# Kernel optimization log

Hardware: AMD Instinct MI355X
Metric: run time of the kernel (lower is better)

The kernel has to match this reference:

```python
import jax, jax.numpy as jnp
import numpy as np

L, H, NH, F = 6, 1024, 16, 4096
B, S = 4, 512
D = H // NH
LN_EPS = 1e-12
GELU_C = 0.7978845608028654  # sqrt(2/pi)


def gelu_new(x):
    return 0.5 * x * (1.0 + jnp.tanh(GELU_C * (x + 0.044715 * x * x * x)))


def layer_norm(x, ln):
    # ln: [2, H] -> gamma, beta
    m = jnp.mean(x, axis=-1, keepdims=True)
    v = jnp.mean(jnp.square(x - m), axis=-1, keepdims=True)
    return (x - m) * jax.lax.rsqrt(v + LN_EPS) * ln[0] + ln[1]


def attention(q_in, kv_in, mask, qkv_w, qkv_b):
    # qkv_w: [3, H, H], qkv_b: [3, H]; mask: [B, S_kv] (1 = keep)
    b, s_q, _ = q_in.shape
    s_kv = kv_in.shape[1]
    q = (q_in @ qkv_w[0] + qkv_b[0]).reshape(b, s_q, NH, D)
    k = (kv_in @ qkv_w[1] + qkv_b[1]).reshape(b, s_kv, NH, D)
    v = (kv_in @ qkv_w[2] + qkv_b[2]).reshape(b, s_kv, NH, D)
    scale = 1.0 / (D ** 0.5)
    score = jnp.einsum('bind,bjnd->bnij', q, k) * scale  # [B, NH, Sq, Skv]
    adder = (1.0 - mask.astype(score.dtype))[:, None, None, :] * -10000.0
    prob = jax.nn.softmax(score + adder, axis=-1)
    out = jnp.einsum('bnij,bjnd->bind', prob, v)
    return out.reshape(b, s_q, H)


def _forward(hidden_states, encoder_hidden_states, attention_mask, encoder_attention_mask,
             sa_qkv_w, sa_qkv_b, sa_out_w, sa_out_b, sa_ln,
             ca_qkv_w, ca_qkv_b, ca_out_w, ca_out_b, ca_ln,
             o1_w, o1_b, o1_ln, ffn_w, ffn_b, o2_w, o2_b, o2_ln):
    h = hidden_states
    for i in range(L):
        # self attention + dense/dropout/LN (residual = h)
        self_vec = attention(h, h, attention_mask, sa_qkv_w[i], sa_qkv_b[i])
        attn_out = layer_norm(self_vec @ sa_out_w[i] + sa_out_b[i] + h, sa_ln[i])
        # cross attention + dense/dropout/LN (residual = h, per original code)
        cross_vec = attention(h, encoder_hidden_states, encoder_attention_mask,
                              ca_qkv_w[i], ca_qkv_b[i])
        cross_out = layer_norm(cross_vec @ ca_out_w[i] + ca_out_b[i] + h, ca_ln[i])
        # output_1: dense(attn_out) + cross_out, then LN
        attn_out = layer_norm(attn_out @ o1_w[i] + o1_b[i] + cross_out, o1_ln[i])
        # FFN with gelu_new, output_2: dense(inter) + attn_out, then LN
        inter = gelu_new(attn_out @ ffn_w[i] + ffn_b[i])
        h = layer_norm(inter @ o2_w[i] + o2_b[i] + attn_out, o2_ln[i])
    return h


def setup_inputs() -> dict:
    key = jax.random.key(0)
    ks = jax.random.split(key, 16)
    std = 0.02
    w = lambda k, shape: (jax.random.normal(k, shape, jnp.float32) * std)
    ln_init = jnp.stack([jnp.ones((L, H), jnp.float32), jnp.zeros((L, H), jnp.float32)], axis=1)
    return {
        'hidden_states': jax.random.normal(ks[0], (B, S, H), jnp.float32),
        'encoder_hidden_states': jax.random.normal(ks[1], (B, S, H), jnp.float32),
        'attention_mask': jnp.ones((B, S), jnp.int32),
        'encoder_attention_mask': jnp.ones((B, S), jnp.int32),
        'sa_qkv_w': w(ks[2], (L, 3, H, H)), 'sa_qkv_b': w(ks[3], (L, 3, H)),
        'sa_out_w': w(ks[4], (L, H, H)), 'sa_out_b': w(ks[5], (L, H)), 'sa_ln': ln_init,
        'ca_qkv_w': w(ks[6], (L, 3, H, H)), 'ca_qkv_b': w(ks[7], (L, 3, H)),
        'ca_out_w': w(ks[8], (L, H, H)), 'ca_out_b': w(ks[9], (L, H)), 'ca_ln': ln_init,
        'o1_w': w(ks[10], (L, H, H)), 'o1_b': w(ks[11], (L, H)), 'o1_ln': ln_init,
        'ffn_w': w(ks[12], (L, H, F)), 'ffn_b': w(ks[13], (L, F)),
        'o2_w': w(ks[14], (L, F, H)), 'o2_b': w(ks[15], (L, H)), 'o2_ln': ln_init,
    }


def reference(hidden_states, encoder_hidden_states, attention_mask, encoder_attention_mask,
              sa_qkv_w, sa_qkv_b, sa_out_w, sa_out_b, sa_ln,
              ca_qkv_w, ca_qkv_b, ca_out_w, ca_out_b, ca_ln,
              o1_w, o1_b, o1_ln, ffn_w, ffn_b, o2_w, o2_b, o2_ln):
    return _forward(hidden_states, encoder_hidden_states, attention_mask, encoder_attention_mask,
                    sa_qkv_w, sa_qkv_b, sa_out_w, sa_out_b, sa_ln,
                    ca_qkv_w, ca_qkv_b, ca_out_w, ca_out_b, ca_ln,
                    o1_w, o1_b, o1_ln, ffn_w, ffn_b, o2_w, o2_b, o2_ln)
```

## Files before the change

kernel.cpp:

```cpp
#include <hip/hip_runtime.h>


#define LNUM 6
#define HDIM 1024
#define NHEAD 16
#define DHEAD 64
#define BDIM 4
#define SDIM 512
#define FDIM 4096
#define MROWS (BDIM * SDIM)
#define HSQ (HDIM * HDIM)

typedef __bf16 bf16_t;
typedef bf16_t bf16x8 __attribute__((ext_vector_type(8)));
typedef float f32x4 __attribute__((ext_vector_type(4)));

__device__ __forceinline__ float bf2f(unsigned short u) {
    union { unsigned int i; float f; } x;
    x.i = ((unsigned int)u) << 16;
    return x.f;
}

__device__ __forceinline__ unsigned short f2bf(float f) {
    union { float f; unsigned int i; } u;
    u.f = f;
    unsigned int x = u.i;
    unsigned int lsb = (x >> 16) & 1u;
    x += 0x7fffu + lsb;
    return (unsigned short)(x >> 16);
}

__device__ __forceinline__ void async16(const unsigned short* g, unsigned short* l) {
    __builtin_amdgcn_global_load_lds(
        (const __attribute__((address_space(1))) unsigned int*)g,
        (__attribute__((address_space(3))) unsigned int*)l, 16, 0, 0);
}

template<int N>
__device__ __forceinline__ void s_wait_vmcnt() {
    asm volatile("s_waitcnt vmcnt(%0)" :: "n"(N) : "memory");
}

template<int BM, int BN, bool GELU, bool OUTBF16>
__global__ __launch_bounds__(256) void mfma_gemm(
    const unsigned short* __restrict__ A,
    const unsigned short* __restrict__ BT,
    const float* __restrict__ bias,
    void* __restrict__ Cv,
    int M, int N, int K)
{
    constexpr int BK = 64;
    constexpr int MI = BM / 32;
    constexpr int NJ = BN / 32;
    constexpr int LPT = MI + NJ;

    __shared__ unsigned short As[3][BM][BK];
    __shared__ unsigned short Bs[3][BN][BK];

    const int t = threadIdx.x;
    const int w = t >> 6;
    const int lane = t & 63;
    const int quad = lane >> 4;
    const int cm = lane & 15;
    const int wrow = (w >> 1) * (BM / 2);
    const int wcol = (w & 1) * (BN / 2);
    const int row0 = blockIdx.x * BM;
    const int col0 = blockIdx.y * BN;

    f32x4 acc[MI][NJ] = {};

    const int lrow = lane >> 3;
    const int lcol = ((lane & 7) ^ lrow) * 8;
    const int sw = cm & 15 & 7;

    auto stage = [&](int buf, int k0) {
#pragma unroll
        for (int j = 0; j < BM / 32; ++j) {
            int mb = w * (BM / 4) + j * 8;
            async16(A + (size_t)(row0 + mb + lrow) * K + k0 + lcol, &As[buf][mb][0]);
        }
#pragma unroll
        for (int j = 0; j < BN / 32; ++j) {
            int nb = w * (BN / 4) + j * 8;
            async16(BT + (size_t)(col0 + nb + lrow) * K + k0 + lcol, &Bs[buf][nb][0]);
        }
    };

    const int NT = K / BK;
    stage(0, 0);
    stage(1, BK);
    int c0 = 0, c1 = 1, c2 = 2;
    for (int ti = 0; ti < NT; ++ti) {
        if (ti + 2 < NT) {
            stage(c2, (ti + 2) * BK);
            s_wait_vmcnt<2 * LPT>();
        } else if (ti + 1 < NT) {
            s_wait_vmcnt<LPT>();
        } else {
            s_wait_vmcnt<0>();
        }
        __builtin_amdgcn_s_barrier();
        __builtin_amdgcn_sched_barrier(0);

#pragma unroll
        for (int kk = 0; kk < BK; kk += 32) {
            const int cc = kk >> 3;
            bf16x8 av[MI], bv[NJ];
#pragma unroll
            for (int i = 0; i < MI; ++i)
                av[i] = *(const bf16x8*)&As[c0][wrow + 16 * i + cm][((cc + quad) ^ sw) * 8];
#pragma unroll
            for (int j = 0; j < NJ; ++j)
                bv[j] = *(const bf16x8*)&Bs[c0][wcol + 16 * j + cm][((cc + quad) ^ sw) * 8];
#pragma unroll
            for (int i = 0; i < MI; ++i)
#pragma unroll
                for (int j = 0; j < NJ; ++j)
                    acc[i][j] = __builtin_amdgcn_mfma_f32_16x16x32_bf16(
                        av[i], bv[j], acc[i][j], 0, 0, 0);
        }

        __builtin_amdgcn_sched_barrier(0);
        __builtin_amdgcn_s_barrier();
        int tmp = c0; c0 = c1; c1 = c2; c2 = tmp;
    }

#pragma unroll
    for (int j = 0; j < NJ; ++j) {
        int col = col0 + wcol + 16 * j + cm;
        float bb = bias[col];
#pragma unroll
        for (int i = 0; i < MI; ++i) {
#pragma unroll
            for (int r = 0; r < 4; ++r) {
                int row = row0 + wrow + 16 * i + quad * 4 + r;
                float c = acc[i][j][r] + bb;
                if (GELU) {
                    float u = 0.7978845608028654f * (c + 0.044715f * c * c * c);
                    c = 0.5f * c * (1.0f + tanhf(u));
                }
                if (OUTBF16)
                    ((unsigned short*)Cv)[(size_t)row * N + col] = f2bf(c);
                else
                    ((float*)Cv)[(size_t)row * N + col] = c;
            }
        }
    }
}

__global__ __launch_bounds__(256) void mfma_gemm_qkv6(
    const unsigned short* __restrict__ hA,
    const unsigned short* __restrict__ encA,
    const unsigned short* __restrict__ swq,
    const unsigned short* __restrict__ cwq,
    const float* __restrict__ sb, const float* __restrict__ cb,
    unsigned short* __restrict__ q1, unsigned short* __restrict__ k1,
    unsigned short* __restrict__ v1,
    unsigned short* __restrict__ q2, unsigned short* __restrict__ k2,
    unsigned short* __restrict__ v2,
    int M, int K)
{
    constexpr int BM = 64, BN = 64, BK = 64;
    constexpr int MI = 2, NJ = 2, LPT = 4;

    __shared__ unsigned short As[3][BM][BK];
    __shared__ unsigned short Bs[3][BN][BK];

    const int t = threadIdx.x;
    const int w = t >> 6;
    const int lane = t & 63;
    const int quad = lane >> 4;
    const int cm = lane & 15;
    const int wrow = (w >> 1) * 32;
    const int wcol = (w & 1) * 32;
    const int row0 = blockIdx.x * BM;
    const int col0 = blockIdx.y * BN;

    const int sec = col0 >> 10;
    const unsigned short* __restrict__ A = (sec <= 3) ? hA : encA;
    const unsigned short* __restrict__ BT =
        (sec < 3) ? swq + (size_t)col0 * K : cwq + (size_t)(col0 - 3072) * K;
    const float* __restrict__ bias = (sec < 3) ? sb + col0 : cb + (col0 - 3072);

    f32x4 acc[MI][NJ] = {};

    const int lrow = lane >> 3;
    const int lcol = ((lane & 7) ^ lrow) * 8;
    const int sw = cm & 7;

    auto stage = [&](int buf, int k0) {
#pragma unroll
        for (int j = 0; j < 2; ++j) {
            int mb = w * 16 + j * 8;
            async16(A + (size_t)(row0 + mb + lrow) * K + k0 + lcol, &As[buf][mb][0]);
        }
#pragma unroll
        for (int j = 0; j < 2; ++j) {
            int nb = w * 16 + j * 8;
            async16(BT + (size_t)(nb + lrow) * K + k0 + lcol, &Bs[buf][nb][0]);
        }
    };

    const int NT = K / BK;
    stage(0, 0);
    stage(1, BK);
    int c0 = 0, c1 = 1, c2 = 2;
    for (int ti = 0; ti < NT; ++ti) {
        if (ti + 2 < NT) {
            stage(c2, (ti + 2) * BK);
            s_wait_vmcnt<2 * LPT>();
        } else if (ti + 1 < NT) {
            s_wait_vmcnt<LPT>();
        } else {
            s_wait_vmcnt<0>();
        }
        __builtin_amdgcn_s_barrier();
        __builtin_amdgcn_sched_barrier(0);

#pragma unroll
        for (int kk = 0; kk < 64; kk += 32) {
            const int cc = kk >> 3;
            bf16x8 av[MI], bv[NJ];
#pragma unroll
            for (int i = 0; i < MI; ++i)
                av[i] = *(const bf16x8*)&As[c0][wrow + 16 * i + cm][((cc + quad) ^ sw) * 8];
#pragma unroll
            for (int j = 0; j < NJ; ++j)
                bv[j] = *(const bf16x8*)&Bs[c0][wcol + 16 * j + cm][((cc + quad) ^ sw) * 8];
#pragma unroll
            for (int i = 0; i < MI; ++i)
#pragma unroll
                for (int j = 0; j < NJ; ++j)
                    acc[i][j] = __builtin_amdgcn_mfma_f32_16x16x32_bf16(
                        av[i], bv[j], acc[i][j], 0, 0, 0);
        }

        __builtin_amdgcn_sched_barrier(0);
        __builtin_amdgcn_s_barrier();
        int tmp = c0; c0 = c1; c1 = c2; c2 = tmp;
    }

    unsigned short* dst = sec == 0 ? q1 : sec == 1 ? k1 : sec == 2 ? v1
                        : sec == 3 ? q2 : sec == 4 ? k2 : v2;
    const int cbase = col0 & 1023;

#pragma unroll
    for (int j = 0; j < NJ; ++j) {
        float bb = bias[wcol + 16 * j + cm];
        int coll = cbase + wcol + 16 * j + cm;
#pragma unroll
        for (int i = 0; i < MI; ++i) {
#pragma unroll
            for (int r = 0; r < 4; ++r) {
                int row = row0 + wrow + 16 * i + quad * 4 + r;
                dst[(size_t)row * HDIM + coll] = f2bf(acc[i][j][r] + bb);
            }
        }
    }
}

__global__ __launch_bounds__(256) void mfma_gemm_out2(
    const unsigned short* __restrict__ A0, const unsigned short* __restrict__ B0,
    const float* __restrict__ b0, float* __restrict__ C0,
    const unsigned short* __restrict__ A1, const unsigned short* __restrict__ B1,
    const float* __restrict__ b1, float* __restrict__ C1,
    int M, int N, int K)
{
    constexpr int BM = 64, BN = 64, BK = 64;
    constexpr int MI = 2, NJ = 2, LPT = 4;

    __shared__ unsigned short As[3][BM][BK];
    __shared__ unsigned short Bs[3][BN][BK];

    const int z = blockIdx.z;
    const unsigned short* __restrict__ A  = z ? A1 : A0;
    const unsigned short* __restrict__ BT = z ? B1 : B0;
    const float* __restrict__ bias = z ? b1 : b0;
    float* __restrict__ Cv = z ? C1 : C0;

    const int t = threadIdx.x;
    const int w = t >> 6;
    const int lane = t & 63;
    const int quad = lane >> 4;
    const int cm = lane & 15;
    const int wrow = (w >> 1) * 32;
    const int wcol = (w & 1) * 32;
    const int row0 = blockIdx.x * BM;
    const int col0 = blockIdx.y * BN;

    f32x4 acc[MI][NJ] = {};

    const int lrow = lane >> 3;
    const int lcol = ((lane & 7) ^ lrow) * 8;
    const int sw = cm & 7;

    auto stage = [&](int buf, int k0) {
#pragma unroll
        for (int j = 0; j < 2; ++j) {
            int mb = w * 16 + j * 8;
            async16(A + (size_t)(row0 + mb + lrow) * K + k0 + lcol, &As[buf][mb][0]);
        }
#pragma unroll
        for (int j = 0; j < 2; ++j) {
            int nb = w * 16 + j * 8;
            async16(BT + (size_t)(col0 + nb + lrow) * K + k0 + lcol, &Bs[buf][nb][0]);
        }
    };

    const int NT = K / BK;
    stage(0, 0);
    stage(1, BK);
    int c0 = 0, c1 = 1, c2 = 2;
    for (int ti = 0; ti < NT; ++ti) {
        if (ti + 2 < NT) {
            stage(c2, (ti + 2) * BK);
            s_wait_vmcnt<2 * LPT>();
        } else if (ti + 1 < NT) {
            s_wait_vmcnt<LPT>();
        } else {
            s_wait_vmcnt<0>();
        }
        __builtin_amdgcn_s_barrier();
        __builtin_amdgcn_sched_barrier(0);

#pragma unroll
        for (int kk = 0; kk < 64; kk += 32) {
            const int cc = kk >> 3;
            bf16x8 av[MI], bv[NJ];
#pragma unroll
            for (int i = 0; i < MI; ++i)
                av[i] = *(const bf16x8*)&As[c0][wrow + 16 * i + cm][((cc + quad) ^ sw) * 8];
#pragma unroll
            for (int j = 0; j < NJ; ++j)
                bv[j] = *(const bf16x8*)&Bs[c0][wcol + 16 * j + cm][((cc + quad) ^ sw) * 8];
#pragma unroll
            for (int i = 0; i < MI; ++i)
#pragma unroll
                for (int j = 0; j < NJ; ++j)
                    acc[i][j] = __builtin_amdgcn_mfma_f32_16x16x32_bf16(
                        av[i], bv[j], acc[i][j], 0, 0, 0);
        }

        __builtin_amdgcn_sched_barrier(0);
        __builtin_amdgcn_s_barrier();
        int tmp = c0; c0 = c1; c1 = c2; c2 = tmp;
    }

#pragma unroll
    for (int j = 0; j < NJ; ++j) {
        int col = col0 + wcol + 16 * j + cm;
        float bb = bias[col];
#pragma unroll
        for (int i = 0; i < MI; ++i) {
#pragma unroll
            for (int r = 0; r < 4; ++r) {
                int row = row0 + wrow + 16 * i + quad * 4 + r;
                Cv[(size_t)row * N + col] = acc[i][j][r] + bb;
            }
        }
    }
}

__global__ __launch_bounds__(256) void flash_attn(
    const unsigned short* __restrict__ q1, const unsigned short* __restrict__ k1,
    const unsigned short* __restrict__ v1,
    const unsigned short* __restrict__ q2, const unsigned short* __restrict__ k2,
    const unsigned short* __restrict__ v2,
    const int* __restrict__ mask1, const int* __restrict__ mask2,
    unsigned short* __restrict__ ctx1, unsigned short* __restrict__ ctx2)
{
    __shared__ unsigned short Qs[64][64];
    __shared__ unsigned short Ks[64][64];
    __shared__ unsigned short Vs[64][72];
    __shared__ unsigned short Ps[4][16][72];

    const int t = threadIdx.x;
    const int w = t >> 6;
    const int lane = t & 63;
    const int quad = lane >> 4;
    const int cm = lane & 15;
    const int sw = cm & 7;

    const int q0 = blockIdx.x * 64;
    const int h = blockIdx.y;
    const int zz = blockIdx.z;
    const int b = zz & (BDIM - 1);
    const int which = zz >> 2;
    const unsigned short* __restrict__ q = which ? q2 : q1;
    const unsigned short* __restrict__ k = which ? k2 : k1;
    const unsigned short* __restrict__ v = which ? v2 : v1;
    const int* __restrict__ mask = which ? mask2 : mask1;
    unsigned short* __restrict__ ctx = which ? ctx2 : ctx1;

    const size_t rowbase = (size_t)b * SDIM;
    const int hoff = h * DHEAD;

#pragma unroll
    for (int l = 0; l < 2; ++l) {
        int idx = t + l * 256;
        int r = idx >> 3;
        int c = idx & 7;
        *(uint4*)&Qs[r][((c ^ (r & 7)) * 8)] =
            *(const uint4*)(q + (rowbase + q0 + r) * HDIM + hoff + c * 8);
    }

    float m_prev[4] = {-1e30f, -1e30f, -1e30f, -1e30f};
    float l_sum[4] = {0.0f, 0.0f, 0.0f, 0.0f};
    f32x4 oacc[4] = {};

    for (int j0 = 0; j0 < SDIM; j0 += 64) {
        __syncthreads();
#pragma unroll
        for (int l = 0; l < 2; ++l) {
            int idx = t + l * 256;
            int r = idx >> 3;
            int c = idx & 7;
            *(uint4*)&Ks[r][((c ^ (r & 7)) * 8)] =
                *(const uint4*)(k + (rowbase + j0 + r) * HDIM + hoff + c * 8);
        }
#pragma unroll
        for (int l = 0; l < 4; ++l) {
            int idx = t + l * 256;
            int jj = idx >> 4;
            int d0 = (idx & 15) * 4;
            ushort4 vv = *(const ushort4*)(v + (rowbase + j0 + jj) * HDIM + hoff + d0);
            Vs[d0 + 0][jj] = vv.x;
            Vs[d0 + 1][jj] = vv.y;
            Vs[d0 + 2][jj] = vv.z;
            Vs[d0 + 3][jj] = vv.w;
        }
        __syncthreads();

        f32x4 sacc[4] = {};
#pragma unroll
        for (int kk = 0; kk < 64; kk += 32) {
            const int cc = kk >> 3;
            bf16x8 av = *(const bf16x8*)&Qs[w * 16 + cm][((cc + quad) ^ sw) * 8];
#pragma unroll
            for (int j2 = 0; j2 < 4; ++j2) {
                bf16x8 bv = *(const bf16x8*)&Ks[j2 * 16 + cm][((cc + quad) ^ sw) * 8];
                sacc[j2] = __builtin_amdgcn_mfma_f32_16x16x32_bf16(av, bv, sacc[j2], 0, 0, 0);
            }
        }

        float madd[4];
#pragma unroll
        for (int j2 = 0; j2 < 4; ++j2)
            madd[j2] = (1.0f - (float)mask[b * SDIM + j0 + j2 * 16 + cm]) * -10000.0f;

#pragma unroll
        for (int r = 0; r < 4; ++r) {
            float s0 = sacc[0][r] * 0.125f + madd[0];
            float s1 = sacc[1][r] * 0.125f + madd[1];
            float s2 = sacc[2][r] * 0.125f + madd[2];
            float s3 = sacc[3][r] * 0.125f + madd[3];
            float rm = fmaxf(fmaxf(s0, s1), fmaxf(s2, s3));
#pragma unroll
            for (int mo = 1; mo < 16; mo <<= 1)
                rm = fmaxf(rm, __shfl_xor(rm, mo, 64));
            float new_m = fmaxf(m_prev[r], rm);
            float alpha = __expf(m_prev[r] - new_m);
            m_prev[r] = new_m;
            float p0 = __expf(s0 - new_m);
            float p1 = __expf(s1 - new_m);
            float p2 = __expf(s2 - new_m);
            float p3 = __expf(s3 - new_m);
            float rs = p0 + p1 + p2 + p3;
#pragma unroll
            for (int mo = 1; mo < 16; mo <<= 1)
                rs += __shfl_xor(rs, mo, 64);
            l_sum[r] = l_sum[r] * alpha + rs;
#pragma unroll
            for (int d2 = 0; d2 < 4; ++d2)
                oacc[d2][r] *= alpha;
            int prow = quad * 4 + r;
            Ps[w][prow][0 * 16 + cm] = f2bf(p0);
            Ps[w][prow][1 * 16 + cm] = f2bf(p1);
            Ps[w][prow][2 * 16 + cm] = f2bf(p2);
            Ps[w][prow][3 * 16 + cm] = f2bf(p3);
        }

#pragma unroll
        for (int kk = 0; kk < 64; kk += 32) {
            bf16x8 pa = *(const bf16x8*)&Ps[w][cm][kk + quad * 8];
#pragma unroll
            for (int d2 = 0; d2 < 4; ++d2) {
                bf16x8 bv = *(const bf16x8*)&Vs[d2 * 16 + cm][kk + quad * 8];
                oacc[d2] = __builtin_amdgcn_mfma_f32_16x16x32_bf16(pa, bv, oacc[d2], 0, 0, 0);
            }
        }
    }

#pragma unroll
    for (int r = 0; r < 4; ++r) {
        float inv = 1.0f / l_sum[r];
        int row = q0 + w * 16 + quad * 4 + r;
#pragma unroll
        for (int d2 = 0; d2 < 4; ++d2) {
            ctx[(rowbase + row) * HDIM + hoff + d2 * 16 + cm] = f2bf(oacc[d2][r] * inv);
        }
    }
}

__global__ __launch_bounds__(256) void convtrans_all(
    const float* __restrict__ sqkv, const float* __restrict__ sout,
    const float* __restrict__ cqkv, const float* __restrict__ cout,
    const float* __restrict__ o1w,  const float* __restrict__ ffnw,
    const float* __restrict__ o2w,
    unsigned short* __restrict__ dq,  unsigned short* __restrict__ dso,
    unsigned short* __restrict__ dcq, unsigned short* __restrict__ dco,
    unsigned short* __restrict__ do1, unsigned short* __restrict__ dffn,
    unsigned short* __restrict__ do2)
{
    __shared__ unsigned short tile[64][72];
    const int bid = blockIdx.x;
    const float* src;
    unsigned short* dst;
    int K, N, tt;
    if (bid < 2304) {
        int m = bid >> 8;
        tt = bid & 255;
        K = HDIM; N = HDIM;
        if (m < 3)      { src = sqkv + (size_t)m * HSQ;       dst = dq  + (size_t)m * HSQ; }
        else if (m < 6) { src = cqkv + (size_t)(m - 3) * HSQ; dst = dcq + (size_t)(m - 3) * HSQ; }
        else if (m == 6){ src = sout; dst = dso; }
        else if (m == 7){ src = cout; dst = dco; }
        else            { src = o1w;  dst = do1; }
    } else if (bid < 3328) {
        tt = bid - 2304; K = HDIM; N = FDIM; src = ffnw; dst = dffn;
    } else {
        tt = bid - 3328; K = FDIM; N = HDIM; src = o2w; dst = do2;
    }
    const int tn = N >> 6;
    const int n0 = (tt % tn) * 64;
    const int k0 = (tt / tn) * 64;
    const int t = threadIdx.x;
#pragma unroll
    for (int l = 0; l < 4; ++l) {
        int idx = t + l * 256;
        int kk = idx >> 4;
        int nn = (idx & 15) * 4;
        float4 v = *(const float4*)(src + (size_t)(k0 + kk) * N + n0 + nn);
        tile[nn + 0][kk] = f2bf(v.x);
        tile[nn + 1][kk] = f2bf(v.y);
        tile[nn + 2][kk] = f2bf(v.z);
        tile[nn + 3][kk] = f2bf(v.w);
    }
    __syncthreads();
#pragma unroll
    for (int l = 0; l < 2; ++l) {
        int c = t + l * 256;
        int nn = c >> 3;
        int kk = (c & 7) * 8;
        *(uint4*)(dst + (size_t)(n0 + nn) * K + k0 + kk) = *(const uint4*)&tile[nn][kk];
    }
}

template<bool OUTF32>
__global__ __launch_bounds__(256) void ln_kernel(
    const float* __restrict__ x, const unsigned short* __restrict__ resid,
    const float* __restrict__ ln, void* __restrict__ out)
{
    const int row = blockIdx.x;
    const float* xr = x + (size_t)row * HDIM;
    const unsigned short* rr = resid + (size_t)row * HDIM;
    const int t = threadIdx.x;
    __shared__ float red[4];

    float4 xv = ((const float4*)xr)[t];
    ushort4 rv = ((const ushort4*)rr)[t];
    float z[4];
    z[0] = xv.x + bf2f(rv.x);
    z[1] = xv.y + bf2f(rv.y);
    z[2] = xv.z + bf2f(rv.z);
    z[3] = xv.w + bf2f(rv.w);
    float s = z[0] + z[1] + z[2] + z[3];
#pragma unroll
    for (int off = 32; off > 0; off >>= 1) s += __shfl_down(s, off, 64);
    if ((t & 63) == 0) red[t >> 6] = s;
    __syncthreads();
    s = red[0] + red[1] + red[2] + red[3];
    float mean = s * (1.0f / (float)HDIM);

    float vs = 0.0f;
#pragma unroll
    for (int i = 0; i < 4; ++i) {
        float d = z[i] - mean;
        vs += d * d;
    }
#pragma unroll
    for (int off = 32; off > 0; off >>= 1) vs += __shfl_down(vs, off, 64);
    __syncthreads();
    if ((t & 63) == 0) red[t >> 6] = vs;
    __syncthreads();
    vs = red[0] + red[1] + red[2] + red[3];
    float inv = rsqrtf(vs * (1.0f / (float)HDIM) + 1e-12f);

    const float* g = ln + 4 * t;
    const float* bb = ln + HDIM + 4 * t;
    if (OUTF32) {
        float4 o;
        o.x = (z[0] - mean) * inv * g[0] + bb[0];
        o.y = (z[1] - mean) * inv * g[1] + bb[1];
        o.z = (z[2] - mean) * inv * g[2] + bb[2];
        o.w = (z[3] - mean) * inv * g[3] + bb[3];
        ((float4*)((float*)out + (size_t)row * HDIM))[t] = o;
    } else {
        ushort4 o;
        o.x = f2bf((z[0] - mean) * inv * g[0] + bb[0]);
        o.y = f2bf((z[1] - mean) * inv * g[1] + bb[1]);
        o.z = f2bf((z[2] - mean) * inv * g[2] + bb[2]);
        o.w = f2bf((z[3] - mean) * inv * g[3] + bb[3]);
        ((ushort4*)((unsigned short*)out + (size_t)row * HDIM))[t] = o;
    }
}

__global__ __launch_bounds__(256) void ln2_kernel(
    const float* __restrict__ xa, const float* __restrict__ xb,
    const unsigned short* __restrict__ resid,
    const float* __restrict__ lna, const float* __restrict__ lnb,
    unsigned short* __restrict__ outa, unsigned short* __restrict__ outb)
{
    const int row = blockIdx.x;
    const int z2 = blockIdx.y;
    const float* x = z2 ? xb : xa;
    const float* ln = z2 ? lnb : lna;
    unsigned short* out = z2 ? outb : outa;

    const float* xr = x + (size_t)row * HDIM;
    const unsigned short* rr = resid + (size_t)row * HDIM;
    const int t = threadIdx.x;
    __shared__ float red[4];

    float4 xv = ((const float4*)xr)[t];
    ushort4 rv = ((const ushort4*)rr)[t];
    float z[4];
    z[0] = xv.x + bf2f(rv.x);
    z[1] = xv.y + bf2f(rv.y);
    z[2] = xv.z + bf2f(rv.z);
    z[3] = xv.w + bf2f(rv.w);
    float s = z[0] + z[1] + z[2] + z[3];
#pragma unroll
    for (int off = 32; off > 0; off >>= 1) s += __shfl_down(s, off, 64);
    if ((t & 63) == 0) red[t >> 6] = s;
    __syncthreads();
    s = red[0] + red[1] + red[2] + red[3];
    float mean = s * (1.0f / (float)HDIM);

    float vs = 0.0f;
#pragma unroll
    for (int i = 0; i < 4; ++i) {
        float d = z[i] - mean;
        vs += d * d;
    }
#pragma unroll
    for (int off = 32; off > 0; off >>= 1) vs += __shfl_down(vs, off, 64);
    __syncthreads();
    if ((t & 63) == 0) red[t >> 6] = vs;
    __syncthreads();
    vs = red[0] + red[1] + red[2] + red[3];
    float inv = rsqrtf(vs * (1.0f / (float)HDIM) + 1e-12f);

    const float* g = ln + 4 * t;
    const float* bb = ln + HDIM + 4 * t;
    ushort4 o;
    o.x = f2bf((z[0] - mean) * inv * g[0] + bb[0]);
    o.y = f2bf((z[1] - mean) * inv * g[1] + bb[1]);
    o.z = f2bf((z[2] - mean) * inv * g[2] + bb[2]);
    o.w = f2bf((z[3] - mean) * inv * g[3] + bb[3]);
    ((ushort4*)(out + (size_t)row * HDIM))[t] = o;
}

__global__ __launch_bounds__(256) void cvt_bf16_kernel(
    const float* __restrict__ in, unsigned short* __restrict__ out, int n4)
{
    int i = blockIdx.x * 256 + threadIdx.x;
    if (i < n4) {
        float4 v = ((const float4*)in)[i];
        ushort4 o;
        o.x = f2bf(v.x); o.y = f2bf(v.y); o.z = f2bf(v.z); o.w = f2bf(v.w);
        ((ushort4*)out)[i] = o;
    }
}

extern "C" void kernel_launch(void* const* d_in, const int* in_sizes, int n_in,
                              void* d_out, int out_size, void* d_ws, size_t ws_size,
                              hipStream_t stream)
{
    const float* in_hidden = (const float*)d_in[0];
    const float* enc_f     = (const float*)d_in[1];
    const int* attn_mask   = (const int*)d_in[2];
    const int* enc_attn_mask = (const int*)d_in[3];
    const float* sa_qkv_w  = (const float*)d_in[4];
    const float* sa_qkv_b  = (const float*)d_in[5];
    const float* sa_out_w  = (const float*)d_in[6];
    const float* sa_out_b  = (const float*)d_in[7];
    const float* sa_ln     = (const float*)d_in[8];
    const float* ca_qkv_w  = (const float*)d_in[9];
    const float* ca_qkv_b  = (const float*)d_in[10];
    const float* ca_out_w  = (const float*)d_in[11];
    const float* ca_out_b  = (const float*)d_in[12];
    const float* ca_ln     = (const float*)d_in[13];
    const float* o1_w      = (const float*)d_in[14];
    const float* o1_b      = (const float*)d_in[15];
    const float* o1_ln     = (const float*)d_in[16];
    const float* ffn_w     = (const float*)d_in[17];
    const float* ffn_b     = (const float*)d_in[18];
    const float* o2_w      = (const float*)d_in[19];
    const float* o2_b      = (const float*)d_in[20];
    const float* o2_ln     = (const float*)d_in[21];

    const size_t MH  = (size_t)MROWS * HDIM;
    const size_t Hsq = (size_t)HDIM * HDIM;
    const size_t HF  = (size_t)HDIM * FDIM;

    char* p = (char*)d_ws;
    unsigned short* wbf = (unsigned short*)p; p += (9 * Hsq + 2 * HF) * 2;
    float* t2a    = (float*)p; p += MH * 4;
    float* t2b    = (float*)p; p += MH * 4;
    unsigned short* qb     = (unsigned short*)p; p += MH * 2;
    unsigned short* kb     = (unsigned short*)p; p += MH * 2;
    unsigned short* vb     = (unsigned short*)p; p += MH * 2;
    unsigned short* qb2    = (unsigned short*)p; p += MH * 2;
    unsigned short* kb2    = (unsigned short*)p; p += MH * 2;
    unsigned short* vb2    = (unsigned short*)p; p += MH * 2;
    unsigned short* ctx    = (unsigned short*)p; p += MH * 2;
    unsigned short* ctx2   = (unsigned short*)p; p += MH * 2;
    unsigned short* h      = (unsigned short*)p; p += MH * 2;
    unsigned short* enc_bf = (unsigned short*)p; p += MH * 2;
    unsigned short* attn1  = (unsigned short*)p; p += MH * 2;
    unsigned short* crossb = (unsigned short*)p; p += MH * 2;
    unsigned short* attn2  = (unsigned short*)p; p += MH * 2;
    unsigned short* tmp8b  = (unsigned short*)p; p += (size_t)MROWS * FDIM * 2;

    unsigned short* w_saqkv = wbf;
    unsigned short* w_saout = wbf + 3 * Hsq;
    unsigned short* w_caqkv = wbf + 4 * Hsq;
    unsigned short* w_caout = wbf + 7 * Hsq;
    unsigned short* w_o1    = wbf + 8 * Hsq;
    unsigned short* w_ffn   = wbf + 9 * Hsq;
    unsigned short* w_o2    = wbf + 9 * Hsq + HF;

    cvt_bf16_kernel<<<(MH / 4 + 255) / 256, 256, 0, stream>>>(in_hidden, h, MH / 4);
    cvt_bf16_kernel<<<(MH / 4 + 255) / 256, 256, 0, stream>>>(enc_f, enc_bf, MH / 4);

    for (int l = 0; l < LNUM; ++l) {
        convtrans_all<<<4352, 256, 0, stream>>>(
            sa_qkv_w + (size_t)l * 3 * Hsq, sa_out_w + (size_t)l * Hsq,
            ca_qkv_w + (size_t)l * 3 * Hsq, ca_out_w + (size_t)l * Hsq,
            o1_w + (size_t)l * Hsq, ffn_w + (size_t)l * HF, o2_w + (size_t)l * HF,
            w_saqkv, w_saout, w_caqkv, w_caout, w_o1, w_ffn, w_o2);

        mfma_gemm_qkv6<<<dim3(MROWS / 64, 6144 / 64), 256, 0, stream>>>(
            h, enc_bf, w_saqkv, w_caqkv,
            sa_qkv_b + (size_t)l * 3 * HDIM, ca_qkv_b + (size_t)l * 3 * HDIM,
            qb, kb, vb, qb2, kb2, vb2, MROWS, HDIM);

        flash_attn<<<dim3(SDIM / 64, NHEAD, 2 * BDIM), 256, 0, stream>>>(
            qb, kb, vb, qb2, kb2, vb2, attn_mask, enc_attn_mask, ctx, ctx2);

        mfma_gemm_out2<<<dim3(MROWS / 64, HDIM / 64, 2), 256, 0, stream>>>(
            ctx, w_saout, sa_out_b + (size_t)l * HDIM, t2a,
            ctx2, w_caout, ca_out_b + (size_t)l * HDIM, t2b,
            MROWS, HDIM, HDIM);

        ln2_kernel<<<dim3(MROWS, 2), 256, 0, stream>>>(
            t2a, t2b, h, sa_ln + (size_t)l * 2 * HDIM, ca_ln + (size_t)l * 2 * HDIM,
            attn1, crossb);

        mfma_gemm<64, 64, false, false><<<dim3(MROWS / 64, HDIM / 64), 256, 0, stream>>>(
            attn1, w_o1, o1_b + (size_t)l * HDIM, t2a, MROWS, HDIM, HDIM);
        ln_kernel<false><<<MROWS, 256, 0, stream>>>(t2a, crossb, o1_ln + (size_t)l * 2 * HDIM, attn2);

        mfma_gemm<64, 128, true, true><<<dim3(MROWS / 64, FDIM / 128), 256, 0, stream>>>(
            attn2, w_ffn, ffn_b + (size_t)l * FDIM, tmp8b, MROWS, FDIM, HDIM);
        mfma_gemm<64, 64, false, false><<<dim3(MROWS / 64, HDIM / 64), 256, 0, stream>>>(
            tmp8b, w_o2, o2_b + (size_t)l * HDIM, t2a, MROWS, HDIM, FDIM);
        if (l == LNUM - 1)
            ln_kernel<true><<<MROWS, 256, 0, stream>>>(
                t2a, attn2, o2_ln + (size_t)l * 2 * HDIM, (float*)d_out);
        else
            ln_kernel<false><<<MROWS, 256, 0, stream>>>(
                t2a, attn2, o2_ln + (size_t)l * 2 * HDIM, h);
    }
}
```

Baseline: 1.786 ms.

## Use 128x128 tiles with 512-thread blocks and split-K for N=1024 GEMMs

```diff
diff --git a/kernel.cpp b/kernel.cpp
--- a/kernel.cpp
+++ b/kernel.cpp
@@ -41,96 +41,104 @@
     asm volatile("s_waitcnt vmcnt(%0)" :: "n"(N) : "memory");
 }
 
-template<int BM, int BN, bool GELU, bool OUTBF16>
-__global__ __launch_bounds__(256) void mfma_gemm(
+__device__ __forceinline__ void gemm128_core(
+    const unsigned short* __restrict__ Abase,
+    const unsigned short* __restrict__ Bbase,
+    int K, int kbeg, int kend,
+    unsigned short (&As)[3][128][64], unsigned short (&Bs)[3][128][64],
+    f32x4 (&acc)[4][2])
+{
+    const int t = threadIdx.x;
+    const int w = t >> 6;
+    const int lane = t & 63;
+    const int quad = lane >> 4;
+    const int cm = lane & 15;
+    const int wrow = (w >> 2) * 64;
+    const int wcol = (w & 3) * 32;
+
+    const int lrow = lane >> 3;
+    const int lcol = ((lane & 7) ^ lrow) * 8;
+    const int sw = cm & 7;
+
+    auto stage = [&](int buf, int k0) {
+#pragma unroll
+        for (int j = 0; j < 2; ++j) {
+            int rb = w * 16 + j * 8;
+            async16(Abase + (size_t)(rb + lrow) * K + k0 + lcol, &As[buf][rb][0]);
+            async16(Bbase + (size_t)(rb + lrow) * K + k0 + lcol, &Bs[buf][rb][0]);
+        }
+    };
+
+    const int NT = (kend - kbeg) / 64;
+    stage(0, kbeg);
+    stage(1, kbeg + 64);
+    int c0 = 0, c1 = 1, c2 = 2;
+    for (int ti = 0; ti < NT; ++ti) {
+        if (ti + 2 < NT) {
+            stage(c2, kbeg + (ti + 2) * 64);
+            s_wait_vmcnt<8>();
+        } else if (ti + 1 < NT) {
+            s_wait_vmcnt<4>();
+        } else {
+            s_wait_vmcnt<0>();
+        }
+        __builtin_amdgcn_s_barrier();
+        __builtin_amdgcn_sched_barrier(0);
+
+#pragma unroll
+        for (int kk = 0; kk < 64; kk += 32) {
+            const int cc = kk >> 3;
+            bf16x8 av[4], bv[2];
+#pragma unroll
+            for (int i = 0; i < 4; ++i)
+                av[i] = *(const bf16x8*)&As[c0][wrow + 16 * i + cm][((cc + quad) ^ sw) * 8];
+#pragma unroll
+            for (int j = 0; j < 2; ++j)
+                bv[j] = *(const bf16x8*)&Bs[c0][wcol + 16 * j + cm][((cc + quad) ^ sw) * 8];
+#pragma unroll
+            for (int i = 0; i < 4; ++i)
+#pragma unroll
+                for (int j = 0; j < 2; ++j)
+                    acc[i][j] = __builtin_amdgcn_mfma_f32_16x16x32_bf16(
+                        av[i], bv[j], acc[i][j], 0, 0, 0);
+        }
+
+        __builtin_amdgcn_sched_barrier(0);
+        __builtin_amdgcn_s_barrier();
+        int tmp = c0; c0 = c1; c1 = c2; c2 = tmp;
+    }
+}
+
+template<bool GELU, bool OUTBF16>
+__global__ __launch_bounds__(512) void gemm128(
     const unsigned short* __restrict__ A,
     const unsigned short* __restrict__ BT,
     const float* __restrict__ bias,
     void* __restrict__ Cv,
     int M, int N, int K)
 {
-    constexpr int BK = 64;
-    constexpr int MI = BM / 32;
-    constexpr int NJ = BN / 32;
-    constexpr int LPT = MI + NJ;
-
-    __shared__ unsigned short As[3][BM][BK];
-    __shared__ unsigned short Bs[3][BN][BK];
-
+    __shared__ unsigned short As[3][128][64];
+    __shared__ unsigned short Bs[3][128][64];
+
+    const int row0 = blockIdx.x * 128;
+    const int col0 = blockIdx.y * 128;
     const int t = threadIdx.x;
     const int w = t >> 6;
     const int lane = t & 63;
     const int quad = lane >> 4;
     const int cm = lane & 15;
-    const int wrow = (w >> 1) * (BM / 2);
-    const int wcol = (w & 1) * (BN / 2);
-    const int row0 = blockIdx.x * BM;
-    const int col0 = blockIdx.y * BN;
-
-    f32x4 acc[MI][NJ] = {};
-
-    const int lrow = lane >> 3;
-    const int lcol = ((lane & 7) ^ lrow) * 8;
-    const int sw = cm & 15 & 7;
-
-    auto stage = [&](int buf, int k0) {
-#pragma unroll
-        for (int j = 0; j < BM / 32; ++j) {
-            int mb = w * (BM / 4) + j * 8;
-            async16(A + (size_t)(row0 + mb + lrow) * K + k0 + lcol, &As[buf][mb][0]);
-        }
-#pragma unroll
-        for (int j = 0; j < BN / 32; ++j) {
-            int nb = w * (BN / 4) + j * 8;
-            async16(BT + (size_t)(col0 + nb + lrow) * K + k0 + lcol, &Bs[buf][nb][0]);
-        }
-    };
-
-    const int NT = K / BK;
-    stage(0, 0);
-    stage(1, BK);
-    int c0 = 0, c1 = 1, c2 = 2;
-    for (int ti = 0; ti < NT; ++ti) {
-        if (ti + 2 < NT) {
-            stage(c2, (ti + 2) * BK);
-            s_wait_vmcnt<2 * LPT>();
-        } else if (ti + 1 < NT) {
-            s_wait_vmcnt<LPT>();
-        } else {
-            s_wait_vmcnt<0>();
-        }
-        __builtin_amdgcn_s_barrier();
-        __builtin_amdgcn_sched_barrier(0);
-
-#pragma unroll
-        for (int kk = 0; kk < BK; kk += 32) {
-            const int cc = kk >> 3;
-            bf16x8 av[MI], bv[NJ];
-#pragma unroll
-            for (int i = 0; i < MI; ++i)
-                av[i] = *(const bf16x8*)&As[c0][wrow + 16 * i + cm][((cc + quad) ^ sw) * 8];
-#pragma unroll
-            for (int j = 0; j < NJ; ++j)
-                bv[j] = *(const bf16x8*)&Bs[c0][wcol + 16 * j + cm][((cc + quad) ^ sw) * 8];
-#pragma unroll
-            for (int i = 0; i < MI; ++i)
-#pragma unroll
-                for (int j = 0; j < NJ; ++j)
-                    acc[i][j] = __builtin_amdgcn_mfma_f32_16x16x32_bf16(
-                        av[i], bv[j], acc[i][j], 0, 0, 0);
-        }
-
-        __builtin_amdgcn_sched_barrier(0);
-        __builtin_amdgcn_s_barrier();
-        int tmp = c0; c0 = c1; c1 = c2; c2 = tmp;
-    }
-
-#pragma unroll
-    for (int j = 0; j < NJ; ++j) {
+    const int wrow = (w >> 2) * 64;
+    const int wcol = (w & 3) * 32;
+
+    f32x4 acc[4][2] = {};
+    gemm128_core(A + (size_t)row0 * K, BT + (size_t)col0 * K, K, 0, K, As, Bs, acc);
+
+#pragma unroll
+    for (int j = 0; j < 2; ++j) {
         int col = col0 + wcol + 16 * j + cm;
         float bb = bias[col];
 #pragma unroll
-        for (int i = 0; i < MI; ++i) {
+        for (int i = 0; i < 4; ++i) {
 #pragma unroll
             for (int r = 0; r < 4; ++r) {
                 int row = row0 + wrow + 16 * i + quad * 4 + r;
@@ -148,7 +156,7 @@
     }
 }
 
-__global__ __launch_bounds__(256) void mfma_gemm_qkv6(
+__global__ __launch_bounds__(512) void gemm128_qkv6(
     const unsigned short* __restrict__ hA,
     const unsigned short* __restrict__ encA,
     const unsigned short* __restrict__ swq,
@@ -160,96 +168,38 @@
     unsigned short* __restrict__ v2,
     int M, int K)
 {
-    constexpr int BM = 64, BN = 64, BK = 64;
-    constexpr int MI = 2, NJ = 2, LPT = 4;
-
-    __shared__ unsigned short As[3][BM][BK];
-    __shared__ unsigned short Bs[3][BN][BK];
-
-    const int t = threadIdx.x;
-    const int w = t >> 6;
-    const int lane = t & 63;
-    const int quad = lane >> 4;
-    const int cm = lane & 15;
-    const int wrow = (w >> 1) * 32;
-    const int wcol = (w & 1) * 32;
-    const int row0 = blockIdx.x * BM;
-    const int col0 = blockIdx.y * BN;
-
+    __shared__ unsigned short As[3][128][64];
+    __shared__ unsigned short Bs[3][128][64];
+
+    const int row0 = blockIdx.x * 128;
+    const int col0 = blockIdx.y * 128;
     const int sec = col0 >> 10;
     const unsigned short* __restrict__ A = (sec <= 3) ? hA : encA;
     const unsigned short* __restrict__ BT =
         (sec < 3) ? swq + (size_t)col0 * K : cwq + (size_t)(col0 - 3072) * K;
     const float* __restrict__ bias = (sec < 3) ? sb + col0 : cb + (col0 - 3072);
 
-    f32x4 acc[MI][NJ] = {};
-
-    const int lrow = lane >> 3;
-    const int lcol = ((lane & 7) ^ lrow) * 8;
-    const int sw = cm & 7;
-
-    auto stage = [&](int buf, int k0) {
-#pragma unroll
-        for (int j = 0; j < 2; ++j) {
-            int mb = w * 16 + j * 8;
-            async16(A + (size_t)(row0 + mb + lrow) * K + k0 + lcol, &As[buf][mb][0]);
-        }
-#pragma unroll
-        for (int j = 0; j < 2; ++j) {
-            int nb = w * 16 + j * 8;
-            async16(BT + (size_t)(nb + lrow) * K + k0 + lcol, &Bs[buf][nb][0]);
-        }
-    };
-
-    const int NT = K / BK;
-    stage(0, 0);
-    stage(1, BK);
-    int c0 = 0, c1 = 1, c2 = 2;
-    for (int ti = 0; ti < NT; ++ti) {
-        if (ti + 2 < NT) {
-            stage(c2, (ti + 2) * BK);
-            s_wait_vmcnt<2 * LPT>();
-        } else if (ti + 1 < NT) {
-            s_wait_vmcnt<LPT>();
-        } else {
-            s_wait_vmcnt<0>();
-        }
-        __builtin_amdgcn_s_barrier();
-        __builtin_amdgcn_sched_barrier(0);
-
-#pragma unroll
-        for (int kk = 0; kk < 64; kk += 32) {
-            const int cc = kk >> 3;
-            bf16x8 av[MI], bv[NJ];
-#pragma unroll
-            for (int i = 0; i < MI; ++i)
-                av[i] = *(const bf16x8*)&As[c0][wrow + 16 * i + cm][((cc + quad) ^ sw) * 8];
-#pragma unroll
-            for (int j = 0; j < NJ; ++j)
-                bv[j] = *(const bf16x8*)&Bs[c0][wcol + 16 * j + cm][((cc + quad) ^ sw) * 8];
-#pragma unroll
-            for (int i = 0; i < MI; ++i)
-#pragma unroll
-                for (int j = 0; j < NJ; ++j)
-                    acc[i][j] = __builtin_amdgcn_mfma_f32_16x16x32_bf16(
-                        av[i], bv[j], acc[i][j], 0, 0, 0);
-        }
-
-        __builtin_amdgcn_sched_barrier(0);
-        __builtin_amdgcn_s_barrier();
-        int tmp = c0; c0 = c1; c1 = c2; c2 = tmp;
-    }
+    const int t = threadIdx.x;
+    const int w = t >> 6;
+    const int lane = t & 63;
+    const int quad = lane >> 4;
+    const int cm = lane & 15;
+    const int wrow = (w >> 2) * 64;
+    const int wcol = (w & 3) * 32;
+
+    f32x4 acc[4][2] = {};
+    gemm128_core(A + (size_t)row0 * K, BT, K, 0, K, As, Bs, acc);
 
     unsigned short* dst = sec == 0 ? q1 : sec == 1 ? k1 : sec == 2 ? v1
                         : sec == 3 ? q2 : sec == 4 ? k2 : v2;
     const int cbase = col0 & 1023;
 
 #pragma unroll
-    for (int j = 0; j < NJ; ++j) {
+    for (int j = 0; j < 2; ++j) {
         float bb = bias[wcol + 16 * j + cm];
         int coll = cbase + wcol + 16 * j + cm;
 #pragma unroll
-        for (int i = 0; i < MI; ++i) {
+        for (int i = 0; i < 4; ++i) {
 #pragma unroll
             for (int r = 0; r < 4; ++r) {
                 int row = row0 + wrow + 16 * i + quad * 4 + r;
@@ -259,18 +209,15 @@
     }
 }
 
-__global__ __launch_bounds__(256) void mfma_gemm_out2(
+__global__ __launch_bounds__(512) void gemm128_out2(
     const unsigned short* __restrict__ A0, const unsigned short* __restrict__ B0,
     const float* __restrict__ b0, float* __restrict__ C0,
     const unsigned short* __restrict__ A1, const unsigned short* __restrict__ B1,
     const float* __restrict__ b1, float* __restrict__ C1,
     int M, int N, int K)
 {
-    constexpr int BM = 64, BN = 64, BK = 64;
-    constexpr int MI = 2, NJ = 2, LPT = 4;
-
-    __shared__ unsigned short As[3][BM][BK];
-    __shared__ unsigned short Bs[3][BN][BK];
+    __shared__ unsigned short As[3][128][64];
+    __shared__ unsigned short Bs[3][128][64];
 
     const int z = blockIdx.z;
     const unsigned short* __restrict__ A  = z ? A1 : A0;
@@ -278,80 +225,67 @@
     const float* __restrict__ bias = z ? b1 : b0;
     float* __restrict__ Cv = z ? C1 : C0;
 
+    const int row0 = blockIdx.x * 128;
+    const int col0 = blockIdx.y * 128;
     const int t = threadIdx.x;
     const int w = t >> 6;
     const int lane = t & 63;
     const int quad = lane >> 4;
     const int cm = lane & 15;
-    const int wrow = (w >> 1) * 32;
-    const int wcol = (w & 1) * 32;
-    const int row0 = blockIdx.x * BM;
-    const int col0 = blockIdx.y * BN;
-
-    f32x4 acc[MI][NJ] = {};
-
-    const int lrow = lane >> 3;
-    const int lcol = ((lane & 7) ^ lrow) * 8;
-    const int sw = cm & 7;
-
-    auto stage = [&](int buf, int k0) {
-#pragma unroll
-        for (int j = 0; j < 2; ++j) {
-            int mb = w * 16 + j * 8;
-            async16(A + (size_t)(row0 + mb + lrow) * K + k0 + lcol, &As[buf][mb][0]);
-        }
-#pragma unroll
-        for (int j = 0; j < 2; ++j) {
-            int nb = w * 16 + j * 8;
-            async16(BT + (size_t)(col0 + nb + lrow) * K + k0 + lcol, &Bs[buf][nb][0]);
-        }
-    };
-
-    const int NT = K / BK;
-    stage(0, 0);
-    stage(1, BK);
-    int c0 = 0, c1 = 1, c2 = 2;
-    for (int ti = 0; ti < NT; ++ti) {
-        if (ti + 2 < NT) {
-            stage(c2, (ti + 2) * BK);
-            s_wait_vmcnt<2 * LPT>();
-        } else if (ti + 1 < NT) {
-            s_wait_vmcnt<LPT>();
-        } else {
-            s_wait_vmcnt<0>();
-        }
-        __builtin_amdgcn_s_barrier();
-        __builtin_amdgcn_sched_barrier(0);
-
-#pragma unroll
-        for (int kk = 0; kk < 64; kk += 32) {
-            const int cc = kk >> 3;
-            bf16x8 av[MI], bv[NJ];
-#pragma unroll
-            for (int i = 0; i < MI; ++i)
-                av[i] = *(const bf16x8*)&As[c0][wrow + 16 * i + cm][((cc + quad) ^ sw) * 8];
-#pragma unroll
-            for (int j = 0; j < NJ; ++j)
-                bv[j] = *(const bf16x8*)&Bs[c0][wcol + 16 * j + cm][((cc + quad) ^ sw) * 8];
-#pragma unroll
-            for (int i = 0; i < MI; ++i)
-#pragma unroll
-                for (int j = 0; j < NJ; ++j)
-                    acc[i][j] = __builtin_amdgcn_mfma_f32_16x16x32_bf16(
-                        av[i], bv[j], acc[i][j], 0, 0, 0);
-        }
-
-        __builtin_amdgcn_sched_barrier(0);
-        __builtin_amdgcn_s_barrier();
-        int tmp = c0; c0 = c1; c1 = c2; c2 = tmp;
-    }
-
-#pragma unroll
-    for (int j = 0; j < NJ; ++j) {
+    const int wrow = (w >> 2) * 64;
+    const int wcol = (w & 3) * 32;
+
+    f32x4 acc[4][2] = {};
+    gemm128_core(A + (size_t)row0 * K, BT + (size_t)col0 * K, K, 0, K, As, Bs, acc);
+
+#pragma unroll
+    for (int j = 0; j < 2; ++j) {
         int col = col0 + wcol + 16 * j + cm;
         float bb = bias[col];
 #pragma unroll
-        for (int i = 0; i < MI; ++i) {
+        for (int i = 0; i < 4; ++i) {
+#pragma unroll
+            for (int r = 0; r < 4; ++r) {
+                int row = row0 + wrow + 16 * i + quad * 4 + r;
+                Cv[(size_t)row * N + col] = acc[i][j][r] + bb;
+            }
+        }
+    }
+}
+
+__global__ __launch_bounds__(512) void gemm128_sk2(
+    const unsigned short* __restrict__ A,
+    const unsigned short* __restrict__ BT,
+    const float* __restrict__ bias,
+    float* __restrict__ C0, float* __restrict__ C1,
+    int M, int N, int K, int Kper)
+{
+    __shared__ unsigned short As[3][128][64];
+    __shared__ unsigned short Bs[3][128][64];
+
+    const int z = blockIdx.z;
+    const int kbeg = z * Kper;
+    const int row0 = blockIdx.x * 128;
+    const int col0 = blockIdx.y * 128;
+    const int t = threadIdx.x;
+    const int w = t >> 6;
+    const int lane = t & 63;
+    const int quad = lane >> 4;
+    const int cm = lane & 15;
+    const int wrow = (w >> 2) * 64;
+    const int wcol = (w & 3) * 32;
+
+    f32x4 acc[4][2] = {};
+    gemm128_core(A + (size_t)row0 * K, BT + (size_t)col0 * K, K,
+                 kbeg, kbeg + Kper, As, Bs, acc);
+
+    float* __restrict__ Cv = z ? C1 : C0;
+#pragma unroll
+    for (int j = 0; j < 2; ++j) {
+        int col = col0 + wcol + 16 * j + cm;
+        float bb = z ? 0.0f : bias[col];
+#pragma unroll
+        for (int i = 0; i < 4; ++i) {
 #pragma unroll
             for (int r = 0; r < 4; ++r) {
                 int row = row0 + wrow + 16 * i + quad * 4 + r;
@@ -556,12 +490,18 @@
     }
 }
 
-template<bool OUTF32>
-__global__ __launch_bounds__(256) void ln_kernel(
-    const float* __restrict__ x, const unsigned short* __restrict__ resid,
-    const float* __restrict__ ln, void* __restrict__ out)
+__global__ __launch_bounds__(256) void ln2_kernel(
+    const float* __restrict__ xa, const float* __restrict__ xb,
+    const unsigned short* __restrict__ resid,
+    const float* __restrict__ lna, const float* __restrict__ lnb,
+    unsigned short* __restrict__ outa, unsigned short* __restrict__ outb)
 {
     const int row = blockIdx.x;
+    const int z2 = blockIdx.y;
+    const float* x = z2 ? xb : xa;
+    const float* ln = z2 ? lnb : lna;
+    unsigned short* out = z2 ? outb : outa;
+
     const float* xr = x + (size_t)row * HDIM;
     const unsigned short* rr = resid + (size_t)row * HDIM;
     const int t = threadIdx.x;
@@ -584,10 +524,57 @@
 
     float vs = 0.0f;
 #pragma unroll
-    for (int i = 0; i < 4; ++i) {
-        float d = z[i] - mean;
-        vs += d * d;
-    }
+    for (int i = 0; i < 4; ++i) { float d = z[i] - mean; vs += d * d; }
+#pragma unroll
+    for (int off = 32; off > 0; off >>= 1) vs += __shfl_down(vs, off, 64);
+    __syncthreads();
+    if ((t & 63) == 0) red[t >> 6] = vs;
+    __syncthreads();
+    vs = red[0] + red[1] + red[2] + red[3];
+    float inv = rsqrtf(vs * (1.0f / (float)HDIM) + 1e-12f);
+
+    const float* g = ln + 4 * t;
+    const float* bb = ln + HDIM + 4 * t;
+    ushort4 o;
+    o.x = f2bf((z[0] - mean) * inv * g[0] + bb[0]);
+    o.y = f2bf((z[1] - mean) * inv * g[1] + bb[1]);
+    o.z = f2bf((z[2] - mean) * inv * g[2] + bb[2]);
+    o.w = f2bf((z[3] - mean) * inv * g[3] + bb[3]);
+    ((ushort4*)(out + (size_t)row * HDIM))[t] = o;
+}
+
+template<bool OUTF32>
+__global__ __launch_bounds__(256) void ln3_kernel(
+    const float* __restrict__ xa, const float* __restrict__ xb,
+    const unsigned short* __restrict__ resid,
+    const float* __restrict__ ln, void* __restrict__ out)
+{
+    const int row = blockIdx.x;
+    const float* xar = xa + (size_t)row * HDIM;
+    const float* xbr = xb + (size_t)row * HDIM;
+    const unsigned short* rr = resid + (size_t)row * HDIM;
+    const int t = threadIdx.x;
+    __shared__ float red[4];
+
+    float4 av = ((const float4*)xar)[t];
+    float4 bv = ((const float4*)xbr)[t];
+    ushort4 rv = ((const ushort4*)rr)[t];
+    float z[4];
+    z[0] = av.x + bv.x + bf2f(rv.x);
+    z[1] = av.y + bv.y + bf2f(rv.y);
+    z[2] = av.z + bv.z + bf2f(rv.z);
+    z[3] = av.w + bv.w + bf2f(rv.w);
+    float s = z[0] + z[1] + z[2] + z[3];
+#pragma unroll
+    for (int off = 32; off > 0; off >>= 1) s += __shfl_down(s, off, 64);
+    if ((t & 63) == 0) red[t >> 6] = s;
+    __syncthreads();
+    s = red[0] + red[1] + red[2] + red[3];
+    float mean = s * (1.0f / (float)HDIM);
+
+    float vs = 0.0f;
+#pragma unroll
+    for (int i = 0; i < 4; ++i) { float d = z[i] - mean; vs += d * d; }
 #pragma unroll
     for (int off = 32; off > 0; off >>= 1) vs += __shfl_down(vs, off, 64);
     __syncthreads();
@@ -613,62 +600,6 @@
         o.w = f2bf((z[3] - mean) * inv * g[3] + bb[3]);
         ((ushort4*)((unsigned short*)out + (size_t)row * HDIM))[t] = o;
     }
-}
-
-__global__ __launch_bounds__(256) void ln2_kernel(
-    const float* __restrict__ xa, const float* __restrict__ xb,
-    const unsigned short* __restrict__ resid,
-    const float* __restrict__ lna, const float* __restrict__ lnb,
-    unsigned short* __restrict__ outa, unsigned short* __restrict__ outb)
-{
-    const int row = blockIdx.x;
-    const int z2 = blockIdx.y;
-    const float* x = z2 ? xb : xa;
-    const float* ln = z2 ? lnb : lna;
-    unsigned short* out = z2 ? outb : outa;
-
-    const float* xr = x + (size_t)row * HDIM;
-    const unsigned short* rr = resid + (size_t)row * HDIM;
-    const int t = threadIdx.x;
-    __shared__ float red[4];
-
-    float4 xv = ((const float4*)xr)[t];
-    ushort4 rv = ((const ushort4*)rr)[t];
-    float z[4];
-    z[0] = xv.x + bf2f(rv.x);
-    z[1] = xv.y + bf2f(rv.y);
-    z[2] = xv.z + bf2f(rv.z);
-    z[3] = xv.w + bf2f(rv.w);
-    float s = z[0] + z[1] + z[2] + z[3];
-#pragma unroll
-    for (int off = 32; off > 0; off >>= 1) s += __shfl_down(s, off, 64);
-    if ((t & 63) == 0) red[t >> 6] = s;
-    __syncthreads();
-    s = red[0] + red[1] + red[2] + red[3];
-    float mean = s * (1.0f / (float)HDIM);
-
-    float vs = 0.0f;
-#pragma unroll
-    for (int i = 0; i < 4; ++i) {
-        float d = z[i] - mean;
-        vs += d * d;
-    }
-#pragma unroll
-    for (int off = 32; off > 0; off >>= 1) vs += __shfl_down(vs, off, 64);
-    __syncthreads();
-    if ((t & 63) == 0) red[t >> 6] = vs;
-    __syncthreads();
-    vs = red[0] + red[1] + red[2] + red[3];
-    float inv = rsqrtf(vs * (1.0f / (float)HDIM) + 1e-12f);
-
-    const float* g = ln + 4 * t;
-    const float* bb = ln + HDIM + 4 * t;
-    ushort4 o;
-    o.x = f2bf((z[0] - mean) * inv * g[0] + bb[0]);
-    o.y = f2bf((z[1] - mean) * inv * g[1] + bb[1]);
-    o.z = f2bf((z[2] - mean) * inv * g[2] + bb[2]);
-    o.w = f2bf((z[3] - mean) * inv * g[3] + bb[3]);
-    ((ushort4*)(out + (size_t)row * HDIM))[t] = o;
 }
 
 __global__ __launch_bounds__(256) void cvt_bf16_kernel(
@@ -751,7 +682,7 @@
             o1_w + (size_t)l * Hsq, ffn_w + (size_t)l * HF, o2_w + (size_t)l * HF,
             w_saqkv, w_saout, w_caqkv, w_caout, w_o1, w_ffn, w_o2);
 
-        mfma_gemm_qkv6<<<dim3(MROWS / 64, 6144 / 64), 256, 0, stream>>>(
+        gemm128_qkv6<<<dim3(MROWS / 128, 6144 / 128), 512, 0, stream>>>(
             h, enc_bf, w_saqkv, w_caqkv,
             sa_qkv_b + (size_t)l * 3 * HDIM, ca_qkv_b + (size_t)l * 3 * HDIM,
             qb, kb, vb, qb2, kb2, vb2, MROWS, HDIM);
@@ -759,7 +690,7 @@
         flash_attn<<<dim3(SDIM / 64, NHEAD, 2 * BDIM), 256, 0, stream>>>(
             qb, kb, vb, qb2, kb2, vb2, attn_mask, enc_attn_mask, ctx, ctx2);
 
-        mfma_gemm_out2<<<dim3(MROWS / 64, HDIM / 64, 2), 256, 0, stream>>>(
+        gemm128_out2<<<dim3(MROWS / 128, HDIM / 128, 2), 512, 0, stream>>>(
             ctx, w_saout, sa_out_b + (size_t)l * HDIM, t2a,
             ctx2, w_caout, ca_out_b + (size_t)l * HDIM, t2b,
             MROWS, HDIM, HDIM);
@@ -768,19 +699,20 @@
             t2a, t2b, h, sa_ln + (size_t)l * 2 * HDIM, ca_ln + (size_t)l * 2 * HDIM,
             attn1, crossb);
 
-        mfma_gemm<64, 64, false, false><<<dim3(MROWS / 64, HDIM / 64), 256, 0, stream>>>(
-            attn1, w_o1, o1_b + (size_t)l * HDIM, t2a, MROWS, HDIM, HDIM);
-        ln_kernel<false><<<MROWS, 256, 0, stream>>>(t2a, crossb, o1_ln + (size_t)l * 2 * HDIM, attn2);
-
-        mfma_gemm<64, 128, true, true><<<dim3(MROWS / 64, FDIM / 128), 256, 0, stream>>>(
+        gemm128_sk2<<<dim3(MROWS / 128, HDIM / 128, 2), 512, 0, stream>>>(
+            attn1, w_o1, o1_b + (size_t)l * HDIM, t2a, t2b, MROWS, HDIM, HDIM, HDIM / 2);
+        ln3_kernel<false><<<MROWS, 256, 0, stream>>>(
+            t2a, t2b, crossb, o1_ln + (size_t)l * 2 * HDIM, attn2);
+
+        gemm128<true, true><<<dim3(MROWS / 128, FDIM / 128), 512, 0, stream>>>(
             attn2, w_ffn, ffn_b + (size_t)l * FDIM, tmp8b, MROWS, FDIM, HDIM);
-        mfma_gemm<64, 64, false, false><<<dim3(MROWS / 64, HDIM / 64), 256, 0, stream>>>(
-            tmp8b, w_o2, o2_b + (size_t)l * HDIM, t2a, MROWS, HDIM, FDIM);
+        gemm128_sk2<<<dim3(MROWS / 128, HDIM / 128, 2), 512, 0, stream>>>(
+            tmp8b, w_o2, o2_b + (size_t)l * HDIM, t2a, t2b, MROWS, HDIM, FDIM, FDIM / 2);
         if (l == LNUM - 1)
-            ln_kernel<true><<<MROWS, 256, 0, stream>>>(
-                t2a, attn2, o2_ln + (size_t)l * 2 * HDIM, (float*)d_out);
+            ln3_kernel<true><<<MROWS, 256, 0, stream>>>(
+                t2a, t2b, attn2, o2_ln + (size_t)l * 2 * HDIM, (float*)d_out);
         else
-            ln_kernel<false><<<MROWS, 256, 0, stream>>>(
-                t2a, attn2, o2_ln + (size_t)l * 2 * HDIM, h);
-    }
-}
+            ln3_kernel<false><<<MROWS, 256, 0, stream>>>(
+                t2a, t2b, attn2, o2_ln + (size_t)l * 2 * HDIM, h);
+    }
+}
```

Measured after the change: 1.780 ms. About the same (-0.3%).
